# Optimization experiments

Hardware: AMD Instinct MI355X
Metric: run time of the kernel (lower is better)

The kernel has to match this reference:

```python
import jax, jax.numpy as jnp
import numpy as np

D_MODEL = 1024
NUM_HEADS = 16
H_DIM = 4096
EPS = 1e-5


def setup_inputs() -> dict:
    key = jax.random.key(0)
    ks = jax.random.split(key, 16)
    B, S, D, H = 2, 2048, D_MODEL, H_DIM
    s = 0.02
    return {
        "x": jax.random.normal(ks[0], (B, S, D), jnp.float32),
        "wq": jax.random.normal(ks[1], (D, D), jnp.float32) * s,
        "bq": jnp.zeros((D,), jnp.float32),
        "wk": jax.random.normal(ks[2], (D, D), jnp.float32) * s,
        "bk": jnp.zeros((D,), jnp.float32),
        "wv": jax.random.normal(ks[3], (D, D), jnp.float32) * s,
        "bv": jnp.zeros((D,), jnp.float32),
        "wo": jax.random.normal(ks[4], (D, D), jnp.float32) * s,
        "bo": jnp.zeros((D,), jnp.float32),
        "ln1_g": jnp.ones((D,), jnp.float32),
        "ln1_b": jnp.zeros((D,), jnp.float32),
        "w1": jax.random.normal(ks[5], (H, D), jnp.float32) * s,
        "b1": jnp.zeros((H,), jnp.float32),
        "w2": jax.random.normal(ks[6], (D, H), jnp.float32) * s,
        "b2": jnp.zeros((D,), jnp.float32),
        "ln2_g": jnp.ones((D,), jnp.float32),
        "ln2_b": jnp.zeros((D,), jnp.float32),
    }


def _layer_norm(x, g, b):
    mu = jnp.mean(x, axis=-1, keepdims=True)
    var = jnp.mean(jnp.square(x - mu), axis=-1, keepdims=True)
    return (x - mu) * jax.lax.rsqrt(var + EPS) * g + b


def _mhsa(x, wq, bq, wk, bk, wv, bv, wo, bo):
    B, S, D = x.shape
    Hh, hd = NUM_HEADS, D // NUM_HEADS
    q = (x @ wq.T + bq).reshape(B, S, Hh, hd)
    k = (x @ wk.T + bk).reshape(B, S, Hh, hd)
    v = (x @ wv.T + bv).reshape(B, S, Hh, hd)
    scale = hd ** -0.5
    scores = jnp.einsum('bqhd,bkhd->bhqk', q, k) * scale
    att = jax.nn.softmax(scores, axis=-1)
    out = jnp.einsum('bhqk,bkhd->bqhd', att, v).reshape(B, S, D)
    return out @ wo.T + bo


def reference(x, wq, bq, wk, bk, wv, bv, wo, bo, ln1_g, ln1_b,
              w1, b1, w2, b2, ln2_g, ln2_b):
    # pre-norm variant as written in the torch source:
    # x = norm1(x); x = x + msa(x)  (residual uses NORMALIZED x)
    x = _layer_norm(x, ln1_g, ln1_b)
    x = x + _mhsa(x, wq, bq, wk, bk, wv, bv, wo, bo)
    x = _layer_norm(x, ln2_g, ln2_b)
    h = jax.nn.gelu(x @ w1.T + b1, approximate=False)
    x = x + (h @ w2.T + b2)
    return x
```

## Files before the change

### kernel.cpp

```cpp
#include <hip/hip_runtime.h>
#include <hip/hip_bf16.h>

typedef unsigned short u16;
typedef __attribute__((ext_vector_type(8))) short short8;
typedef __attribute__((ext_vector_type(4))) float f32x4;

#define DM 1024
#define HM 4096
#define NHEADS 16
#define HD 64
#define SQ 2048
#define NBATCH 2
#define NTOK 4096

#define NX  ((size_t)NTOK * DM)

__device__ __forceinline__ u16 f2b(float f) {
    union { float f; unsigned int i; } w; w.f = f;
    unsigned int x = w.i;
    return (u16)((x + 0x7FFFu + ((x >> 16) & 1u)) >> 16);
}
__device__ __forceinline__ u16 f2b_ru(float f) {
    union { float f; unsigned int i; } w; w.f = f;
    return (u16)((w.i + 0x8000u) >> 16);
}

__device__ __forceinline__ void gload_lds16(const void* g, void* l) {
    __builtin_amdgcn_global_load_lds(
        (const __attribute__((address_space(1))) void*)g,
        (__attribute__((address_space(3))) void*)l, 16, 0, 0);
}

__global__ void cvt_all(const float* __restrict__ wq, const float* __restrict__ wk,
                        const float* __restrict__ wv, const float* __restrict__ wo,
                        const float* __restrict__ w1, const float* __restrict__ w2,
                        const float* __restrict__ bq, const float* __restrict__ bk,
                        const float* __restrict__ bv, float* __restrict__ bias_dst,
                        u16* __restrict__ dst) {
    const int NW4 = DM * DM / 4;
    int i = blockIdx.x * 256 + threadIdx.x;
    if (i < 12 * NW4) {
        const float* src; int base; float sc = 1.0f;
        if      (i <     NW4) { src = wq; base = 0;       sc = 0.125f; }
        else if (i < 2 * NW4) { src = wk; base = NW4; }
        else if (i < 3 * NW4) { src = wv; base = 2 * NW4; }
        else if (i < 4 * NW4) { src = wo; base = 3 * NW4; }
        else if (i < 8 * NW4) { src = w1; base = 4 * NW4; }
        else                  { src = w2; base = 8 * NW4; }
        float4 f = ((const float4*)src)[i - base];
        ushort4 o;
        o.x = f2b(f.x * sc); o.y = f2b(f.y * sc);
        o.z = f2b(f.z * sc); o.w = f2b(f.w * sc);
        ((ushort4*)dst)[i] = o;
    } else {
        int j = i - 12 * NW4;
        if (j < 3 * DM) {
            float v = (j < DM) ? bq[j] * 0.125f
                    : (j < 2 * DM) ? bk[j - DM] : bv[j - 2 * DM];
            bias_dst[j] = v;
        }
    }
}

__global__ void ln_kernel(const float* __restrict__ xin, const float* __restrict__ g,
                          const float* __restrict__ b, float* __restrict__ outf,
                          u16* __restrict__ outb) {
    int t = blockIdx.x, tid = threadIdx.x;
    float4 f = ((const float4*)(xin + (size_t)t * DM))[tid];
    float v0 = f.x, v1 = f.y, v2 = f.z, v3 = f.w;
    float s  = v0 + v1 + v2 + v3;
    float ss = v0*v0 + v1*v1 + v2*v2 + v3*v3;
    #pragma unroll
    for (int o = 32; o > 0; o >>= 1) {
        s  += __shfl_down(s,  o, 64);
        ss += __shfl_down(ss, o, 64);
    }
    __shared__ float rs[4], rss[4];
    int w = tid >> 6, lane = tid & 63;
    if (!lane) { rs[w] = s; rss[w] = ss; }
    __syncthreads();
    s  = rs[0] + rs[1] + rs[2] + rs[3];
    ss = rss[0] + rss[1] + rss[2] + rss[3];
    float mean = s * (1.0f / DM);
    float var  = ss * (1.0f / DM) - mean * mean;
    float rstd = rsqrtf(var + 1e-5f);
    float4 gu = ((const float4*)g)[tid];
    float4 bu = ((const float4*)b)[tid];
    float4 o;
    o.x = (v0 - mean) * rstd * gu.x + bu.x;
    o.y = (v1 - mean) * rstd * gu.y + bu.y;
    o.z = (v2 - mean) * rstd * gu.z + bu.z;
    o.w = (v3 - mean) * rstd * gu.w + bu.w;
    ((float4*)(outf + (size_t)t * DM))[tid] = o;
    ushort4 ob; ob.x = f2b(o.x); ob.y = f2b(o.y); ob.z = f2b(o.z); ob.w = f2b(o.w);
    ((ushort4*)(outb + (size_t)t * DM))[tid] = ob;
}

__global__ void vtr_kernel(const u16* __restrict__ qkv, u16* __restrict__ vT) {
    __shared__ u16 tile[64][72];
    int bid = blockIdx.x;
    int tt = bid & 31, bh = bid >> 5;
    int h = bh & (NHEADS - 1), b = bh >> 4;
    int tid = threadIdx.x;
    int r = tid >> 2, c0 = (tid & 3) << 4;
    const u16* src = qkv + ((size_t)(b * SQ + tt * 64 + r)) * (3 * DM) + 2 * DM + h * HD + c0;
    #pragma unroll
    for (int j = 0; j < 4; j++)
        *(ushort4*)&tile[r][c0 + (j << 2)] = *(const ushort4*)(src + (j << 2));
    __syncthreads();
    int dd = tid >> 2, t0 = (tid & 3) << 4;
    u16* dst = vT + ((size_t)bh * HD + dd) * SQ + tt * 64 + t0;
    #pragma unroll
    for (int j = 0; j < 4; j++) {
        ushort4 v;
        v.x = tile[t0 + (j << 2) + 0][dd];
        v.y = tile[t0 + (j << 2) + 1][dd];
        v.z = tile[t0 + (j << 2) + 2][dd];
        v.w = tile[t0 + (j << 2) + 3][dd];
        *(ushort4*)(dst + (j << 2)) = v;
    }
}

template<int GELU, int RESID, int OUTBF>
__global__ __launch_bounds__(256, 2)
void gemm_bt(const u16* __restrict__ A, const u16* __restrict__ W,
             const float* __restrict__ bias, const float* __restrict__ resid,
             void* __restrict__ Cout, int M, int N, int K) {
    __shared__ __attribute__((aligned(16))) u16 As[2 * 128 * 64];
    __shared__ __attribute__((aligned(16))) u16 Bs[2 * 128 * 64];
    int tid  = threadIdx.x;
    int wid  = tid >> 6, lane = tid & 63;
    int m0 = blockIdx.y << 7, n0 = blockIdx.x << 7;
    int wm = (wid & 1) << 6, wn = (wid >> 1) << 6;

    int rIn = lane >> 3;
    int cSw = (((lane & 7) ^ (lane >> 3)) << 3);
    int s0  = wid << 2;
    int fr = lane & 15;
    int ksw0 = (((lane >> 4) ^ (lane & 7)) << 3);
    int ksw1 = (((4 + (lane >> 4)) ^ (lane & 7)) << 3);

    f32x4 acc[4][4];
    #pragma unroll
    for (int i = 0; i < 4; i++)
        #pragma unroll
        for (int j = 0; j < 4; j++)
            acc[i][j] = (f32x4){0.f, 0.f, 0.f, 0.f};

    #pragma unroll
    for (int t = 0; t < 4; t++) {
        int s = s0 + t;
        gload_lds16(A + (size_t)(m0 + (s << 3) + rIn) * K + cSw, As + (s << 9));
        gload_lds16(W + (size_t)(n0 + (s << 3) + rIn) * K + cSw, Bs + (s << 9));
    }
    __syncthreads();

    int nk = K >> 6;
    for (int kt = 0; kt < nk; kt++) {
        int buf = kt & 1;
        const u16* Ab = As + (buf << 13);
        const u16* Bb = Bs + (buf << 13);
        if (kt + 1 < nk) {
            int k0 = (kt + 1) << 6;
            int bo = (buf ^ 1) << 13;
            #pragma unroll
            for (int t = 0; t < 4; t++) {
                int s = s0 + t;
                gload_lds16(A + (size_t)(m0 + (s << 3) + rIn) * K + k0 + cSw, As + bo + (s << 9));
                gload_lds16(W + (size_t)(n0 + (s << 3) + rIn) * K + k0 + cSw, Bs + bo + (s << 9));
            }
        }
        #pragma unroll
        for (int ch = 0; ch < 2; ch++) {
            int ks = ch ? ksw1 : ksw0;
            short8 af[4], bf[4];
            #pragma unroll
            for (int mi = 0; mi < 4; mi++)
                af[mi] = *(const short8*)(Ab + (size_t)(wm + (mi << 4) + fr) * 64 + ks);
            #pragma unroll
            for (int ni = 0; ni < 4; ni++)
                bf[ni] = *(const short8*)(Bb + (size_t)(wn + (ni << 4) + fr) * 64 + ks);
            #pragma unroll
            for (int mi = 0; mi < 4; mi++)
                #pragma unroll
                for (int ni = 0; ni < 4; ni++)
                    acc[mi][ni] = __builtin_amdgcn_mfma_f32_16x16x32_bf16(
                        af[mi], bf[ni], acc[mi][ni], 0, 0, 0);
        }
        __syncthreads();
    }

    int erow = (lane >> 4) << 2;
    #pragma unroll
    for (int ni = 0; ni < 4; ni++) {
        int col = n0 + wn + (ni << 4) + fr;
        float bv = bias[col];
        #pragma unroll
        for (int mi = 0; mi < 4; mi++) {
            #pragma unroll
            for (int r = 0; r < 4; r++) {
                int row = m0 + wm + (mi << 4) + erow + r;
                float val = acc[mi][ni][r] + bv;
                if (GELU)  val = 0.5f * val * (1.0f + erff(val * 0.70710678118654752f));
                if (RESID) val += resid[(size_t)row * N + col];
                if (OUTBF) ((u16*)Cout)[(size_t)row * N + col] = f2b(val);
                else       ((float*)Cout)[(size_t)row * N + col] = val;
            }
        }
    }
}

template<int GELU, int RESID, int OUTBF>
__global__ __launch_bounds__(256, 3)
void gemm_n64(const u16* __restrict__ A, const u16* __restrict__ W,
              const float* __restrict__ bias, const float* __restrict__ resid,
              void* __restrict__ Cout, int M, int N, int K) {
    __shared__ __attribute__((aligned(16))) u16 As[2 * 128 * 64];
    __shared__ __attribute__((aligned(16))) u16 Bs[2 * 64 * 64];
    int tid  = threadIdx.x;
    int wid  = tid >> 6, lane = tid & 63;
    int m0 = blockIdx.y << 7, n0 = blockIdx.x << 6;
    int wm = (wid & 1) << 6, wn = (wid >> 1) << 5;

    int rIn = lane >> 3;
    int cSw = (((lane & 7) ^ (lane >> 3)) << 3);
    int sA = wid << 2;
    int sB = wid << 1;
    int fr = lane & 15;
    int ksw0 = (((lane >> 4) ^ (lane & 7)) << 3);
    int ksw1 = (((4 + (lane >> 4)) ^ (lane & 7)) << 3);

    f32x4 acc[4][2];
    #pragma unroll
    for (int i = 0; i < 4; i++)
        #pragma unroll
        for (int j = 0; j < 2; j++)
            acc[i][j] = (f32x4){0.f, 0.f, 0.f, 0.f};

    #pragma unroll
    for (int t = 0; t < 4; t++) {
        int s = sA + t;
        gload_lds16(A + (size_t)(m0 + (s << 3) + rIn) * K + cSw, As + (s << 9));
    }
    #pragma unroll
    for (int t = 0; t < 2; t++) {
        int s = sB + t;
        gload_lds16(W + (size_t)(n0 + (s << 3) + rIn) * K + cSw, Bs + (s << 9));
    }
    __syncthreads();

    int nk = K >> 6;
    for (int kt = 0; kt < nk; kt++) {
        int buf = kt & 1;
        const u16* Ab = As + (buf << 13);
        const u16* Bb = Bs + (buf << 12);
        if (kt + 1 < nk) {
            int k0 = (kt + 1) << 6;
            int boA = (buf ^ 1) << 13;
            int boB = (buf ^ 1) << 12;
            #pragma unroll
            for (int t = 0; t < 4; t++) {
                int s = sA + t;
                gload_lds16(A + (size_t)(m0 + (s << 3) + rIn) * K + k0 + cSw, As + boA + (s << 9));
            }
            #pragma unroll
            for (int t = 0; t < 2; t++) {
                int s = sB + t;
                gload_lds16(W + (size_t)(n0 + (s << 3) + rIn) * K + k0 + cSw, Bs + boB + (s << 9));
            }
        }
        #pragma unroll
        for (int ch = 0; ch < 2; ch++) {
            int ks = ch ? ksw1 : ksw0;
            short8 af[4], bf[2];
            #pragma unroll
            for (int mi = 0; mi < 4; mi++)
                af[mi] = *(const short8*)(Ab + (size_t)(wm + (mi << 4) + fr) * 64 + ks);
            #pragma unroll
            for (int ni = 0; ni < 2; ni++)
                bf[ni] = *(const short8*)(Bb + (size_t)(wn + (ni << 4) + fr) * 64 + ks);
            #pragma unroll
            for (int mi = 0; mi < 4; mi++)
                #pragma unroll
                for (int ni = 0; ni < 2; ni++)
                    acc[mi][ni] = __builtin_amdgcn_mfma_f32_16x16x32_bf16(
                        af[mi], bf[ni], acc[mi][ni], 0, 0, 0);
        }
        __syncthreads();
    }

    int erow = (lane >> 4) << 2;
    #pragma unroll
    for (int ni = 0; ni < 2; ni++) {
        int col = n0 + wn + (ni << 4) + fr;
        float bv = bias[col];
        #pragma unroll
        for (int mi = 0; mi < 4; mi++) {
            #pragma unroll
            for (int r = 0; r < 4; r++) {
                int row = m0 + wm + (mi << 4) + erow + r;
                float val = acc[mi][ni][r] + bv;
                if (GELU)  val = 0.5f * val * (1.0f + erff(val * 0.70710678118654752f));
                if (RESID) val += resid[(size_t)row * N + col];
                if (OUTBF) ((u16*)Cout)[(size_t)row * N + col] = f2b(val);
                else       ((float*)Cout)[(size_t)row * N + col] = val;
            }
        }
    }
}

__global__ __launch_bounds__(256) void fattn_mfma(const u16* __restrict__ QKV,
                                                  const u16* __restrict__ VT,
                                                  u16* __restrict__ O) {
    __shared__ __attribute__((aligned(16))) u16 QP[4096];
    __shared__ __attribute__((aligned(16))) u16 Ks[2][4096];
    __shared__ __attribute__((aligned(16))) u16 Vt[2][4096];
    const int ld = 3 * DM;
    int bid = blockIdx.x;
    int qt = bid & 31, bh = bid >> 5;
    int h = bh & (NHEADS - 1), b = bh >> 4;
    int tid = threadIdx.x, wid = tid >> 6, lane = tid & 63;
    int fr = lane & 15;
    int fcs = (((lane >> 4) ^ ((fr >> 1) & 3)) << 3);
    int lsw = (((lane & 3) ^ ((lane >> 3) & 3)) << 3);
    size_t tokb = (size_t)b * SQ;
    const u16* Qg  = QKV + tokb * ld + h * HD;
    const u16* Kg  = QKV + tokb * ld + DM + h * HD;
    const u16* VTg = VT + ((size_t)bh * HD) * SQ;
    int s0 = wid << 1;
    u16* Ps = QP + (wid << 10);

    {
        #pragma unroll
        for (int t = 0; t < 2; t++) {
            int s = s0 + t;
            const u16* g = Qg + (size_t)(qt * 64 + ((s & 3) << 4) + (lane >> 2)) * ld
                         + ((s >> 2) << 5) + lsw;
            gload_lds16(g, QP + (s << 9));
        }
    }
    {
        #pragma unroll
        for (int t = 0; t < 2; t++) {
            int s = s0 + t;
            const u16* g = Kg + (size_t)(((s & 3) << 4) + (lane >> 2)) * ld
                         + ((s >> 2) << 5) + lsw;
            gload_lds16(g, Ks[0] + (s << 9));
            const u16* gv = VTg + (size_t)(((s & 3) << 4) + (lane >> 2)) * SQ
                          + ((s >> 2) << 5) + lsw;
            gload_lds16(gv, Vt[0] + (s << 9));
        }
    }
    f32x4 oacc[4];
    #pragma unroll
    for (int di = 0; di < 4; di++) oacc[di] = (f32x4){0.f, 0.f, 0.f, 0.f};
    float lsum[4] = {0.f, 0.f, 0.f, 0.f};
    __syncthreads();
    short8 aq0 = *(const short8*)(QP + ((wid << 4) + fr) * 32 + fcs);
    short8 aq1 = *(const short8*)(QP + 2048 + ((wid << 4) + fr) * 32 + fcs);
    __syncthreads();

    for (int kt = 0; kt < SQ / 64; kt++) {
        int buf = kt & 1;
        if (kt + 1 < SQ / 64) {
            #pragma unroll
            for (int t = 0; t < 2; t++) {
                int s = s0 + t;
                const u16* g = Kg + (size_t)((kt + 1) * 64 + ((s & 3) << 4) + (lane >> 2)) * ld
                             + ((s >> 2) << 5) + lsw;
                gload_lds16(g, Ks[buf ^ 1] + (s << 9));
                const u16* gv = VTg + (size_t)(((s & 3) << 4) + (lane >> 2)) * SQ
                              + (kt + 1) * 64 + ((s >> 2) << 5) + lsw;
                gload_lds16(gv, Vt[buf ^ 1] + (s << 9));
            }
        }
        #pragma unroll
        for (int ni = 0; ni < 4; ni++) {
            short8 bk0 = *(const short8*)(Ks[buf] + ((ni << 4) + fr) * 32 + fcs);
            short8 bk1 = *(const short8*)(Ks[buf] + 2048 + ((ni << 4) + fr) * 32 + fcs);
            f32x4 z = (f32x4){0.f, 0.f, 0.f, 0.f};
            __builtin_amdgcn_s_setprio(1);
            z = __builtin_amdgcn_mfma_f32_16x16x32_bf16(aq0, bk0, z, 0, 0, 0);
            z = __builtin_amdgcn_mfma_f32_16x16x32_bf16(aq1, bk1, z, 0, 0, 0);
            __builtin_amdgcn_s_setprio(0);
            int c  = (ni << 4) + fr;
            int cb = (c >> 5) << 9;
            int khi = (c & 31) >> 3, klo = c & 7;
            #pragma unroll
            for (int r = 0; r < 4; r++) {
                float e = __expf(z[r]);
                lsum[r] += e;
                int row = ((lane >> 4) << 2) + r;
                Ps[cb + row * 32 + ((khi ^ ((row >> 1) & 3)) << 3) + klo] = f2b_ru(e);
            }
        }
        short8 ap0 = *(const short8*)(Ps + fr * 32 + fcs);
        short8 ap1 = *(const short8*)(Ps + 512 + fr * 32 + fcs);
        __builtin_amdgcn_s_setprio(1);
        #pragma unroll
        for (int di = 0; di < 4; di++) {
            short8 bv0 = *(const short8*)(Vt[buf] + ((di << 4) + fr) * 32 + fcs);
            short8 bv1 = *(const short8*)(Vt[buf] + 2048 + ((di << 4) + fr) * 32 + fcs);
            oacc[di] = __builtin_amdgcn_mfma_f32_16x16x32_bf16(ap0, bv0, oacc[di], 0, 0, 0);
            oacc[di] = __builtin_amdgcn_mfma_f32_16x16x32_bf16(ap1, bv1, oacc[di], 0, 0, 0);
        }
        __builtin_amdgcn_s_setprio(0);
        __syncthreads();
    }
    #pragma unroll
    for (int msk = 1; msk <= 8; msk <<= 1)
        #pragma unroll
        for (int r = 0; r < 4; r++) lsum[r] += __shfl_xor(lsum[r], msk, 64);
    float inv[4];
    #pragma unroll
    for (int r = 0; r < 4; r++) inv[r] = 1.0f / lsum[r];
    #pragma unroll
    for (int di = 0; di < 4; di++) {
        int d = (di << 4) + fr;
        #pragma unroll
        for (int r = 0; r < 4; r++) {
            int q = qt * 64 + (wid << 4) + ((lane >> 4) << 2) + r;
            O[(tokb + q) * DM + h * HD + d] = f2b(oacc[di][r] * inv[r]);
        }
    }
}

extern "C" void kernel_launch(void* const* d_in, const int* in_sizes, int n_in,
                              void* d_out, int out_size, void* d_ws, size_t ws_size,
                              hipStream_t stream) {
    if (n_in < 17) return;
    const float* x   = (const float*)d_in[0];
    const float* wq  = (const float*)d_in[1];
    const float* bq  = (const float*)d_in[2];
    const float* wk  = (const float*)d_in[3];
    const float* bk  = (const float*)d_in[4];
    const float* wv  = (const float*)d_in[5];
    const float* bv  = (const float*)d_in[6];
    const float* wo  = (const float*)d_in[7];
    const float* bo  = (const float*)d_in[8];
    const float* g1  = (const float*)d_in[9];
    const float* e1  = (const float*)d_in[10];
    const float* w1  = (const float*)d_in[11];
    const float* b1  = (const float*)d_in[12];
    const float* w2  = (const float*)d_in[13];
    const float* b2  = (const float*)d_in[14];
    const float* g2  = (const float*)d_in[15];
    const float* e2  = (const float*)d_in[16];

    float* F = (float*)d_ws;
    size_t off = 0;
    float* xnf   = F + off; off += NX;
    u16*   xnb   = (u16*)(F + off); off += NX / 2;
    u16*   qkvb  = (u16*)(F + off); off += (size_t)NTOK * 3 * DM / 2;
    u16*   vTb   = (u16*)(F + off); off += (size_t)NTOK * DM / 2;
    float* y     = F + off; off += NX;
    u16*   aob   = (u16*)(F + off); off += NX / 2;
    u16*   hb    = (u16*)(F + off); off += (size_t)NTOK * HM / 2;
    u16*   wqkvb = (u16*)(F + off); off += (size_t)3 * DM * DM / 2;
    u16*   wob   = (u16*)(F + off); off += (size_t)DM * DM / 2;
    u16*   w1b   = (u16*)(F + off); off += (size_t)HM * DM / 2;
    u16*   w2b   = (u16*)(F + off); off += (size_t)DM * HM / 2;
    float* bqkv  = F + off; off += 3 * DM;
    if (ws_size < off * sizeof(float)) return;

    dim3 blk(256);
    cvt_all<<<(12 * DM * DM / 4 + 3 * DM + 255) / 256, blk, 0, stream>>>(
        wq, wk, wv, wo, w1, w2, bq, bk, bv, bqkv, wqkvb);

    ln_kernel<<<NTOK, blk, 0, stream>>>(x, g1, e1, xnf, xnb);
    gemm_bt<0,0,1><<<dim3(3 * DM / 128, NTOK / 128), blk, 0, stream>>>(
        xnb, wqkvb, bqkv, nullptr, qkvb, NTOK, 3 * DM, DM);
    vtr_kernel<<<NBATCH * NHEADS * (SQ / 64), blk, 0, stream>>>(qkvb, vTb);
    fattn_mfma<<<NBATCH * NHEADS * (SQ / 64), blk, 0, stream>>>(qkvb, vTb, aob);
    gemm_n64<0,1,0><<<dim3(DM / 64, NTOK / 128), blk, 0, stream>>>(
        aob, wob, bo, xnf, y, NTOK, DM, DM);
    ln_kernel<<<NTOK, blk, 0, stream>>>(y, g2, e2, xnf, xnb);
    gemm_bt<1,0,1><<<dim3(HM / 128, NTOK / 128), blk, 0, stream>>>(
        xnb, w1b, b1, nullptr, hb, NTOK, HM, DM);
    gemm_n64<0,1,0><<<dim3(DM / 64, NTOK / 128), blk, 0, stream>>>(
        hb, w2b, b2, xnf, d_out, NTOK, DM, HM);
}
```

Before: 386.9 us.

## Keep attention probabilities in registers via transposed QK MFMA and lane shuffles

Computes S^T by swapping the MFMA operands so each lane holds probabilities for one query row. The probabilities are packed to bf16 with v_cvt_pk_bf16_f32 and rearranged into the PV A-operand layout with cross-lane shuffles, instead of a round trip through LDS. This removes the LDS write/read of P and a __syncthreads, and simplifies the row-sum reduction. In exchange it adds 16 shuffles per tile, and the bf16 rounding changes from round-up to the hardware conversion.

```diff
diff --git a/kernel.cpp b/kernel.cpp
--- a/kernel.cpp
+++ b/kernel.cpp
@@ -19,10 +19,6 @@
     union { float f; unsigned int i; } w; w.f = f;
     unsigned int x = w.i;
     return (u16)((x + 0x7FFFu + ((x >> 16) & 1u)) >> 16);
-}
-__device__ __forceinline__ u16 f2b_ru(float f) {
-    union { float f; unsigned int i; } w; w.f = f;
-    return (u16)((w.i + 0x8000u) >> 16);
 }
 
 __device__ __forceinline__ void gload_lds16(const void* g, void* l) {
@@ -323,12 +319,14 @@
     int fr = lane & 15;
     int fcs = (((lane >> 4) ^ ((fr >> 1) & 3)) << 3);
     int lsw = (((lane & 3) ^ ((lane >> 3) & 3)) << 3);
+    int i0 = fr + ((lane & 16) << 1);
+    int i1 = i0 + 16;
+    bool loHalf = (lane < 32);
     size_t tokb = (size_t)b * SQ;
     const u16* Qg  = QKV + tokb * ld + h * HD;
     const u16* Kg  = QKV + tokb * ld + DM + h * HD;
     const u16* VTg = VT + ((size_t)bh * HD) * SQ;
     int s0 = wid << 1;
-    u16* Ps = QP + (wid << 10);
 
     {
         #pragma unroll
@@ -354,11 +352,10 @@
     f32x4 oacc[4];
     #pragma unroll
     for (int di = 0; di < 4; di++) oacc[di] = (f32x4){0.f, 0.f, 0.f, 0.f};
-    float lsum[4] = {0.f, 0.f, 0.f, 0.f};
+    float lsum = 0.f;
     __syncthreads();
     short8 aq0 = *(const short8*)(QP + ((wid << 4) + fr) * 32 + fcs);
     short8 aq1 = *(const short8*)(QP + 2048 + ((wid << 4) + fr) * 32 + fcs);
-    __syncthreads();
 
     for (int kt = 0; kt < SQ / 64; kt++) {
         int buf = kt & 1;
@@ -374,28 +371,41 @@
                 gload_lds16(gv, Vt[buf ^ 1] + (s << 9));
             }
         }
+        float p[4][4];
         #pragma unroll
         for (int ni = 0; ni < 4; ni++) {
             short8 bk0 = *(const short8*)(Ks[buf] + ((ni << 4) + fr) * 32 + fcs);
             short8 bk1 = *(const short8*)(Ks[buf] + 2048 + ((ni << 4) + fr) * 32 + fcs);
             f32x4 z = (f32x4){0.f, 0.f, 0.f, 0.f};
             __builtin_amdgcn_s_setprio(1);
-            z = __builtin_amdgcn_mfma_f32_16x16x32_bf16(aq0, bk0, z, 0, 0, 0);
-            z = __builtin_amdgcn_mfma_f32_16x16x32_bf16(aq1, bk1, z, 0, 0, 0);
+            z = __builtin_amdgcn_mfma_f32_16x16x32_bf16(bk0, aq0, z, 0, 0, 0);
+            z = __builtin_amdgcn_mfma_f32_16x16x32_bf16(bk1, aq1, z, 0, 0, 0);
             __builtin_amdgcn_s_setprio(0);
-            int c  = (ni << 4) + fr;
-            int cb = (c >> 5) << 9;
-            int khi = (c & 31) >> 3, klo = c & 7;
             #pragma unroll
             for (int r = 0; r < 4; r++) {
                 float e = __expf(z[r]);
-                lsum[r] += e;
-                int row = ((lane >> 4) << 2) + r;
-                Ps[cb + row * 32 + ((khi ^ ((row >> 1) & 3)) << 3) + klo] = f2b_ru(e);
-            }
-        }
-        short8 ap0 = *(const short8*)(Ps + fr * 32 + fcs);
-        short8 ap1 = *(const short8*)(Ps + 512 + fr * 32 + fcs);
+                lsum += e;
+                p[ni][r] = e;
+            }
+        }
+        unsigned int W[4][2];
+        #pragma unroll
+        for (int ni = 0; ni < 4; ni++) {
+            asm("v_cvt_pk_bf16_f32 %0, %1, %2" : "=v"(W[ni][0]) : "v"(p[ni][0]), "v"(p[ni][1]));
+            asm("v_cvt_pk_bf16_f32 %0, %1, %2" : "=v"(W[ni][1]) : "v"(p[ni][2]), "v"(p[ni][3]));
+        }
+        union { unsigned int w[4]; short8 v; } fA0, fA1;
+        #pragma unroll
+        for (int jp = 0; jp < 4; jp++) {
+            int idx = (jp >= 2) ? i1 : i0;
+            int a0 = __shfl((int)W[0][jp & 1], idx, 64);
+            int a1 = __shfl((int)W[1][jp & 1], idx, 64);
+            fA0.w[jp] = loHalf ? (unsigned)a0 : (unsigned)a1;
+            int b0 = __shfl((int)W[2][jp & 1], idx, 64);
+            int b1 = __shfl((int)W[3][jp & 1], idx, 64);
+            fA1.w[jp] = loHalf ? (unsigned)b0 : (unsigned)b1;
+        }
+        short8 ap0 = fA0.v, ap1 = fA1.v;
         __builtin_amdgcn_s_setprio(1);
         #pragma unroll
         for (int di = 0; di < 4; di++) {
@@ -407,20 +417,20 @@
         __builtin_amdgcn_s_setprio(0);
         __syncthreads();
     }
-    #pragma unroll
-    for (int msk = 1; msk <= 8; msk <<= 1)
-        #pragma unroll
-        for (int r = 0; r < 4; r++) lsum[r] += __shfl_xor(lsum[r], msk, 64);
-    float inv[4];
-    #pragma unroll
-    for (int r = 0; r < 4; r++) inv[r] = 1.0f / lsum[r];
+    lsum += __shfl_xor(lsum, 16, 64);
+    lsum += __shfl_xor(lsum, 32, 64);
+    float inv = 1.0f / lsum;
+    float invq[4];
+    #pragma unroll
+    for (int r = 0; r < 4; r++)
+        invq[r] = __shfl(inv, ((lane >> 4) << 2) + r, 64);
     #pragma unroll
     for (int di = 0; di < 4; di++) {
         int d = (di << 4) + fr;
         #pragma unroll
         for (int r = 0; r < 4; r++) {
             int q = qt * 64 + (wid << 4) + ((lane >> 4) << 2) + r;
-            O[(tokb + q) * DM + h * HD + d] = f2b(oacc[di][r] * inv[r]);
+            O[(tokb + q) * DM + h * HD + d] = f2b(oacc[di][r] * invq[r]);
         }
     }
 }
```

After: 391.2 us. Within noise of the previous version (+1.1%).
